# Kernel tuning notes

Hardware: AMD Instinct MI355X
Metric: run time of the kernel (lower is better)

The kernel has to match this reference:

```python
import jax, jax.numpy as jnp
import numpy as np

B, V, N, C, H = 4, 8, 256, 768, 12
DH = C // H
NEG = -1e9


def setup_inputs() -> dict:
    key = jax.random.key(0)
    k0, k1, k2, k3, k4, k5 = jax.random.split(key, 6)
    feats = jax.random.normal(k0, (B, V, N, C), dtype=jnp.float32)
    is_ref = jax.random.randint(k1, (B, V), 0, 2).astype(bool)
    # nn.MultiheadAttention params: packed in_proj (3C, C) + bias, out_proj Linear(C, C)
    w_qkv = jax.random.normal(k2, (3 * C, C), dtype=jnp.float32) * 0.02
    b_qkv = jax.random.normal(k3, (3 * C,), dtype=jnp.float32) * 0.02
    w_out = jax.random.normal(k4, (C, C), dtype=jnp.float32) * 0.02
    b_out = jax.random.normal(k5, (C,), dtype=jnp.float32) * 0.02
    return {"feats": feats, "is_ref": is_ref, "w_qkv": w_qkv, "b_qkv": b_qkv,
            "w_out": w_out, "b_out": b_out}


def reference(feats, is_ref, w_qkv, b_qkv, w_out, b_out):
    b_, v_, n_, c_ = feats.shape
    # packed QKV projection (torch Linear: x @ W.T + b)
    qkv = feats @ w_qkv.T + b_qkv                      # (B,V,N,3C)
    q, k, v = jnp.split(qkv, 3, axis=-1)
    q = q.reshape(b_, v_, n_, H, DH) * (1.0 / jnp.sqrt(jnp.float32(DH)))
    k = k.reshape(b_, v_ * n_, H, DH)                  # keys flattened over views
    v = v.reshape(b_, v_ * n_, H, DH)
    # view v attends to views w with opposite ref flag
    allowed = is_ref[:, :, None] ^ is_ref[:, None, :]  # (B,V,V) bool
    key_mask = jnp.repeat(allowed, n_, axis=2)         # (B,V,V*N)
    scores = jnp.einsum('bvnhd,bmhd->bhvnm', q, k)     # (B,H,V,N,V*N)
    logits = jnp.where(key_mask[:, None, :, None, :], scores, NEG)
    attn = jax.nn.softmax(logits, axis=-1)
    ctx = jnp.einsum('bhvnm,bmhd->bvnhd', attn, v).reshape(b_, v_, n_, c_)
    out = ctx @ w_out.T + b_out
    # views with empty context pass through unchanged
    has_ctx = allowed.any(axis=-1)                     # (B,V)
    return jnp.where(has_ctx[:, :, None, None], out, feats)
```

## Files before the change

### kernel.cpp

```cpp
#include <hip/hip_runtime.h>
#include <hip/hip_bf16.h>
#include <math.h>

#define BDIM 4
#define VDIM 8
#define NDIM 256
#define CDIM 768
#define HDIM 12
#define DHE  64
#define C3   (3*CDIM)
#define ROWS (BDIM*VDIM*NDIM)
#define KEYS (VDIM*NDIM)

typedef __attribute__((ext_vector_type(8))) short short8;
typedef __attribute__((ext_vector_type(4))) float float4v;

__device__ inline unsigned short f2bf(float f) {
    unsigned int u = __builtin_bit_cast(unsigned int, f);
    u += 0x7fffu + ((u >> 16) & 1u);
    return (unsigned short)(u >> 16);
}

__device__ __forceinline__ unsigned int pk2(float a, float b) {
    return (unsigned int)f2bf(a) | ((unsigned int)f2bf(b) << 16);
}

__device__ __forceinline__ uint4 pk8(float4 a, float4 b) {
    uint4 r;
    r.x = pk2(a.x, a.y); r.y = pk2(a.z, a.w);
    r.z = pk2(b.x, b.y); r.w = pk2(b.z, b.w);
    return r;
}

__device__ __forceinline__ void gld_lds16(const unsigned short* g, unsigned short* l) {
    __builtin_amdgcn_global_load_lds(
        (const __attribute__((address_space(1))) void*)g,
        (__attribute__((address_space(3))) void*)l, 16, 0, 0);
}

#define NA8 786432
#define NW8 221184
#define NO8 73728

__global__ __launch_bounds__(256) void cast_bf16_all(
    const float* __restrict__ fA, const float* __restrict__ fW,
    const float* __restrict__ fO,
    unsigned short* __restrict__ bA, unsigned short* __restrict__ bW,
    unsigned short* __restrict__ bO)
{
    const int gid = blockIdx.x * 256 + threadIdx.x;
    const float* src;
    unsigned short* dst;
    int idx;
    if (gid < NA8)            { src = fA; dst = bA; idx = gid; }
    else if (gid < NA8 + NW8) { src = fW; dst = bW; idx = gid - NA8; }
    else                      { src = fO; dst = bO; idx = gid - NA8 - NW8; }
    const float4* p = (const float4*)(src + (size_t)idx * 8);
    *(uint4*)(dst + (size_t)idx * 8) = pk8(p[0], p[1]);
}

__global__ __launch_bounds__(256) void gemm_qkv_mfma(
    const unsigned short* __restrict__ A,
    const unsigned short* __restrict__ W,
    const float* __restrict__ bias,
    unsigned short* __restrict__ out,
    unsigned short* __restrict__ vT)
{
    __shared__ __attribute__((aligned(16))) unsigned short As[128][32];
    __shared__ __attribute__((aligned(16))) unsigned short Ws[128][32];
    const int t = threadIdx.x;
    const int wave = t >> 6, lane = t & 63;
    const int m = lane & 15, quad = lane >> 4;
    const int wr = (wave >> 1) * 64, wc = (wave & 1) * 64;
    const int row0 = blockIdx.y * 128, col0 = blockIdx.x * 128;

    const int sr = t >> 2, sk = (t & 3) * 8;
    const unsigned short* ag = &A[(size_t)(row0 + sr) * CDIM + sk];
    const unsigned short* wg = &W[(size_t)(col0 + sr) * CDIM + sk];
    unsigned short* la0 = &As[sr][sk];
    unsigned short* la1 = &As[64 + sr][sk];
    unsigned short* lw0 = &Ws[sr][sk];
    unsigned short* lw1 = &Ws[64 + sr][sk];

    float4v acc[4][4] = {};

    for (int k0 = 0; k0 < CDIM; k0 += 32) {
        gld_lds16(ag + k0, la0);
        gld_lds16(ag + (size_t)64 * CDIM + k0, la1);
        gld_lds16(wg + k0, lw0);
        gld_lds16(wg + (size_t)64 * CDIM + k0, lw1);
        __syncthreads();
        short8 a[4], b[4];
        #pragma unroll
        for (int rt = 0; rt < 4; rt++)
            a[rt] = *(const short8*)&As[wr + rt * 16 + m][quad * 8];
        #pragma unroll
        for (int ct = 0; ct < 4; ct++)
            b[ct] = *(const short8*)&Ws[wc + ct * 16 + m][quad * 8];
        #pragma unroll
        for (int rt = 0; rt < 4; rt++)
            #pragma unroll
            for (int ct = 0; ct < 4; ct++)
                acc[rt][ct] = __builtin_amdgcn_mfma_f32_16x16x32_bf16(
                    a[rt], b[ct], acc[rt][ct], 0, 0, 0);
        __syncthreads();
    }

    if (col0 < 2 * CDIM) {
        #pragma unroll
        for (int ct = 0; ct < 4; ct++) {
            const int col = col0 + wc + ct * 16 + m;
            const float bv = bias[col];
            #pragma unroll
            for (int rt = 0; rt < 4; rt++) {
                const size_t row = (size_t)row0 + wr + rt * 16 + quad * 4;
                #pragma unroll
                for (int r = 0; r < 4; r++)
                    out[(row + r) * C3 + col] = f2bf(acc[rt][ct][r] + bv);
            }
        }
    } else {
        #pragma unroll
        for (int ct = 0; ct < 4; ct++) {
            const int vcol = col0 + wc + ct * 16 + m - 2 * CDIM;
            const int h = vcol >> 6, d = vcol & 63;
            const float bv = bias[col0 + wc + ct * 16 + m];
            #pragma unroll
            for (int rt = 0; rt < 4; rt++) {
                const int row = row0 + wr + rt * 16 + quad * 4;
                const int bidx = row >> 11, key = row & 2047;
                ushort4 pkv;
                pkv.x = f2bf(acc[rt][ct][0] + bv);
                pkv.y = f2bf(acc[rt][ct][1] + bv);
                pkv.z = f2bf(acc[rt][ct][2] + bv);
                pkv.w = f2bf(acc[rt][ct][3] + bv);
                *(ushort4*)&vT[((size_t)(bidx * HDIM + h) * DHE + d) * KEYS + key] = pkv;
            }
        }
    }
}

__global__ __launch_bounds__(256, 3) void attn_mfma(
    const unsigned short* __restrict__ qkv,
    const unsigned short* __restrict__ vT,
    const int* __restrict__ is_ref,
    unsigned short* __restrict__ ctx)
{
    const int g = blockIdx.x;
    const int myx = g & 7, cuu = (g >> 3) & 31, round = g >> 8;
    const int j = round * 32 + ((round & 1) ? (31 - cuu) : cuu);

    int rmask[4], r4[4];
    #pragma unroll
    for (int bb = 0; bb < 4; bb++) {
        int mask = 0;
        #pragma unroll
        for (int w = 0; w < VDIM; w++)
            if (is_ref[bb * VDIM + w] != 0) mask |= 1 << w;
        rmask[bb] = mask; r4[bb] = __popc(mask);
    }
    int ord[4] = {0, 1, 2, 3};
    #pragma unroll
    for (int i = 0; i < 3; i++)
        #pragma unroll
        for (int k = 0; k < 3 - i; k++) {
            const int wa = r4[ord[k]] * (8 - r4[ord[k]]);
            const int wb = r4[ord[k + 1]] * (8 - r4[ord[k + 1]]);
            if (wb > wa) { int tmp = ord[k]; ord[k] = ord[k + 1]; ord[k + 1] = tmp; }
        }
    int Gb[6], Gh[6], ng = 0;
    for (int p = 0; p < 48; p++) {
        const int row = p >> 3, col = p & 7;
        const int x = (row & 1) ? (7 - col) : col;
        if (x == myx) { Gb[ng] = ord[p / 12]; Gh[ng] = p % 12; ng++; }
    }
    int b = 0, h = 0, half = 0, v = 0, Lsel = 0;
    {
        int jj = j;
        bool found = false;
        for (int o = 8; o >= 0 && !found; o--) {
            for (int gi = 0; gi < 6 && !found; gi++) {
                const int b2 = Gb[gi], r2 = r4[b2];
                const int nv_o = ((8 - r2) == o ? r2 : 0) + (r2 == o ? (8 - r2) : 0);
                const int cnt = 2 * nv_o;
                if (cnt > 0 && jj < cnt) {
                    b = b2; h = Gh[gi]; Lsel = o;
                    half = jj / nv_o;
                    int pos = jj % nv_o;
                    int S = (((8 - r2) == o) ? rmask[b2] : 0)
                          | ((r2 == o) ? ((~rmask[b2]) & 0xff) : 0);
                    for (int vv = 0; vv < 8; vv++)
                        if ((S >> vv) & 1) { if (pos == 0) { v = vv; break; } pos--; }
                    found = true;
                } else jj -= cnt;
            }
        }
    }

    const int t = threadIdx.x, wave = t >> 6, lane = t & 63;
    const int m = lane & 15, quad = lane >> 4;
    const int n0 = half * 128 + wave * 32;

    __shared__ unsigned short Ks[128][64];
    __shared__ unsigned short Vs[64][128];
    __shared__ unsigned short Ps[4][32][72];

    const int my_ref = (rmask[b] >> v) & 1;
    const unsigned amask = my_ref ? (unsigned)((~rmask[b]) & 0xff)
                                  : (unsigned)rmask[b];
    const int nChunks = 2 * Lsel;

    const float c1 = 0.18033688f;

    short8 aq[2][2];
    #pragma unroll
    for (int qt = 0; qt < 2; qt++) {
        const size_t row = (size_t)((b * VDIM + v) * NDIM) + n0 + qt * 16 + m;
        #pragma unroll
        for (int ks = 0; ks < 2; ks++)
            aq[qt][ks] = *(const short8*)&qkv[row * C3 + h * DHE + ks * 32 + quad * 8];
    }

    float rs[2] = {0.f, 0.f};
    float4v O[2][4] = {};

    const int k_key = t >> 3, k_dg = t & 7;
    const int v_dim = t >> 4, v_kg = t & 15;

    const unsigned short* vTb = vT + (size_t)(b * HDIM + h) * DHE * KEYS;

    uint4 kreg[4], vreg[4];
    unsigned rem2 = amask;
    int wcur = __builtin_ffs((int)rem2) - 1;

    if (nChunks > 0) {
        const unsigned short* kb =
            qkv + (size_t)((b * VDIM + wcur) * NDIM) * C3 + CDIM + h * DHE;
        #pragma unroll
        for (int i = 0; i < 4; i++)
            kreg[i] = *(const uint4*)&kb[(size_t)(i * 32 + k_key) * C3 + k_dg * 8];
        #pragma unroll
        for (int i = 0; i < 4; i++)
            vreg[i] = *(const uint4*)&vTb[(size_t)(i * 16 + v_dim) * KEYS
                                          + wcur * NDIM + v_kg * 8];
    }

    for (int ci = 0; ci < nChunks; ci++) {
        __syncthreads();
        #pragma unroll
        for (int i = 0; i < 4; i++)
            *(uint4*)&Ks[i * 32 + k_key][(k_dg ^ (k_key & 7)) * 8] = kreg[i];
        #pragma unroll
        for (int i = 0; i < 4; i++)
            *(uint4*)&Vs[i * 16 + v_dim][(v_kg ^ v_dim) * 8] = vreg[i];

        if (ci + 1 < nChunks) {
            int wn, m0n;
            if ((ci & 1) == 0) { wn = wcur; m0n = 128; }
            else {
                unsigned r2 = rem2 & (rem2 - 1);
                wn = __builtin_ffs((int)r2) - 1; m0n = 0;
            }
            const unsigned short* kb =
                qkv + (size_t)((b * VDIM + wn) * NDIM + m0n) * C3 + CDIM + h * DHE;
            #pragma unroll
            for (int i = 0; i < 4; i++)
                kreg[i] = *(const uint4*)&kb[(size_t)(i * 32 + k_key) * C3 + k_dg * 8];
            #pragma unroll
            for (int i = 0; i < 4; i++)
                vreg[i] = *(const uint4*)&vTb[(size_t)(i * 16 + v_dim) * KEYS
                                              + wn * NDIM + m0n + v_kg * 8];
        }
        __syncthreads();

        #pragma unroll
        for (int hk = 0; hk < 2; hk++) {
            #pragma unroll
            for (int kt = 0; kt < 4; kt++) {
                const int nt = hk * 4 + kt;
                const short8 bk0 = *(const short8*)&Ks[nt * 16 + m][(quad ^ (m & 7)) * 8];
                const short8 bk1 = *(const short8*)&Ks[nt * 16 + m][((4 + quad) ^ (m & 7)) * 8];
                #pragma unroll
                for (int qt = 0; qt < 2; qt++) {
                    float4v s = {};
                    s = __builtin_amdgcn_mfma_f32_16x16x32_bf16(bk0, aq[qt][0], s, 0, 0, 0);
                    s = __builtin_amdgcn_mfma_f32_16x16x32_bf16(bk1, aq[qt][1], s, 0, 0, 0);
                    const float p0 = __builtin_amdgcn_exp2f(s[0] * c1);
                    const float p1 = __builtin_amdgcn_exp2f(s[1] * c1);
                    const float p2 = __builtin_amdgcn_exp2f(s[2] * c1);
                    const float p3 = __builtin_amdgcn_exp2f(s[3] * c1);
                    rs[qt] += (p0 + p1) + (p2 + p3);
                    uint2 pw;
                    pw.x = pk2(p0, p1);
                    pw.y = pk2(p2, p3);
                    *(uint2*)&Ps[wave][qt * 16 + m][kt * 16 + quad * 4] = pw;
                }
            }
            #pragma unroll
            for (int kk = 0; kk < 2; kk++) {
                const short8 ap0 = *(const short8*)&Ps[wave][m][kk * 32 + quad * 8];
                const short8 ap1 = *(const short8*)&Ps[wave][16 + m][kk * 32 + quad * 8];
                #pragma unroll
                for (int ct = 0; ct < 4; ct++) {
                    const short8 bv = *(const short8*)&Vs[ct * 16 + m]
                        [((hk * 8 + kk * 4 + quad) ^ m) * 8];
                    O[0][ct] = __builtin_amdgcn_mfma_f32_16x16x32_bf16(ap0, bv, O[0][ct], 0, 0, 0);
                    O[1][ct] = __builtin_amdgcn_mfma_f32_16x16x32_bf16(ap1, bv, O[1][ct], 0, 0, 0);
                }
            }
        }
        if (ci & 1) { rem2 &= rem2 - 1; wcur = __builtin_ffs((int)rem2) - 1; }
    }

    #pragma unroll
    for (int qt = 0; qt < 2; qt++) {
        float x = rs[qt];
        x += __shfl_xor(x, 16, 64);
        x += __shfl_xor(x, 32, 64);
        const float inv = (x > 0.f) ? 1.f / x : 0.f;
        float invq[4];
        #pragma unroll
        for (int r = 0; r < 4; r++)
            invq[r] = __shfl(inv, quad * 4 + r, 64);
        const size_t rowg = (size_t)((b * VDIM + v) * NDIM) + n0 + qt * 16 + quad * 4;
        #pragma unroll
        for (int ct = 0; ct < 4; ct++)
            #pragma unroll
            for (int r = 0; r < 4; r++)
                ctx[(rowg + r) * CDIM + h * DHE + ct * 16 + m] = f2bf(O[qt][ct][r] * invq[r]);
    }
}

__global__ __launch_bounds__(256) void gemm_out_mfma(
    const unsigned short* __restrict__ A,
    const unsigned short* __restrict__ W,
    const float* __restrict__ bias,
    const float* __restrict__ feats,
    const int* __restrict__ is_ref,
    float* __restrict__ out)
{
    __shared__ __attribute__((aligned(16))) unsigned short As[128][32];
    __shared__ __attribute__((aligned(16))) unsigned short Ws[128][32];
    const int t = threadIdx.x;
    const int wave = t >> 6, lane = t & 63;
    const int m = lane & 15, quad = lane >> 4;
    const int wr = (wave >> 1) * 64, wc = (wave & 1) * 64;
    const int row0 = blockIdx.y * 128, col0 = blockIdx.x * 128;

    const int sr = t >> 2, sk = (t & 3) * 8;
    const unsigned short* ag = &A[(size_t)(row0 + sr) * CDIM + sk];
    const unsigned short* wg = &W[(size_t)(col0 + sr) * CDIM + sk];
    unsigned short* la0 = &As[sr][sk];
    unsigned short* la1 = &As[64 + sr][sk];
    unsigned short* lw0 = &Ws[sr][sk];
    unsigned short* lw1 = &Ws[64 + sr][sk];

    float4v acc[4][4] = {};

    for (int k0 = 0; k0 < CDIM; k0 += 32) {
        gld_lds16(ag + k0, la0);
        gld_lds16(ag + (size_t)64 * CDIM + k0, la1);
        gld_lds16(wg + k0, lw0);
        gld_lds16(wg + (size_t)64 * CDIM + k0, lw1);
        __syncthreads();
        short8 a[4], b[4];
        #pragma unroll
        for (int rt = 0; rt < 4; rt++)
            a[rt] = *(const short8*)&As[wr + rt * 16 + m][quad * 8];
        #pragma unroll
        for (int ct = 0; ct < 4; ct++)
            b[ct] = *(const short8*)&Ws[wc + ct * 16 + m][quad * 8];
        #pragma unroll
        for (int rt = 0; rt < 4; rt++)
            #pragma unroll
            for (int ct = 0; ct < 4; ct++)
                acc[rt][ct] = __builtin_amdgcn_mfma_f32_16x16x32_bf16(
                    a[rt], b[ct], acc[rt][ct], 0, 0, 0);
        __syncthreads();
    }

    const int bidx = row0 / (VDIM * NDIM);
    const int vidx = (row0 / NDIM) % VDIM;
    const int my = is_ref[bidx * VDIM + vidx];
    bool has = false;
    #pragma unroll
    for (int w = 0; w < VDIM; w++) has = has || (is_ref[bidx * VDIM + w] != my);

    #pragma unroll
    for (int ct = 0; ct < 4; ct++) {
        const int col = col0 + wc + ct * 16 + m;
        const float bv = bias[col];
        #pragma unroll
        for (int rt = 0; rt < 4; rt++) {
            const size_t row = (size_t)row0 + wr + rt * 16 + quad * 4;
            #pragma unroll
            for (int r = 0; r < 4; r++) {
                float o = acc[rt][ct][r] + bv;
                if (!has) o = feats[(row + r) * CDIM + col];
                out[(row + r) * CDIM + col] = o;
            }
        }
    }
}

extern "C" void kernel_launch(void* const* d_in, const int* in_sizes, int n_in,
                              void* d_out, int out_size, void* d_ws, size_t ws_size,
                              hipStream_t stream) {
    const float* feats = (const float*)d_in[0];
    const int*   is_ref = (const int*)d_in[1];
    const float* w_qkv = (const float*)d_in[2];
    const float* b_qkv = (const float*)d_in[3];
    const float* w_out = (const float*)d_in[4];
    const float* b_out = (const float*)d_in[5];
    float* out = (float*)d_out;

    unsigned short* qkv_b = (unsigned short*)d_ws;
    unsigned short* vT    = qkv_b + (size_t)ROWS * C3;
    unsigned short* ctx_b = vT + (size_t)BDIM * HDIM * DHE * KEYS;
    unsigned short* A_bf  = ctx_b + (size_t)ROWS * CDIM;
    unsigned short* Wq_bf = A_bf + (size_t)ROWS * CDIM;
    unsigned short* Wo_bf = Wq_bf + (size_t)C3 * CDIM;

    cast_bf16_all<<<dim3((NA8 + NW8 + NO8) / 256), 256, 0, stream>>>(
        feats, w_qkv, w_out, A_bf, Wq_bf, Wo_bf);

    dim3 g1(C3 / 128, ROWS / 128);
    gemm_qkv_mfma<<<g1, 256, 0, stream>>>(A_bf, Wq_bf, b_qkv, qkv_b, vT);

    attn_mfma<<<dim3(768), 256, 0, stream>>>(qkv_b, vT, is_ref, ctx_b);

    dim3 g3(CDIM / 128, ROWS / 128);
    gemm_out_mfma<<<g3, 256, 0, stream>>>(ctx_b, Wo_bf, b_out, feats, is_ref, out);
    (void)in_sizes; (void)n_in; (void)out_size; (void)ws_size;
}
```

Before: 245.9 us.

## Swizzle GEMM block order per XCD and pass P via lane shuffles instead of LDS

```diff
diff --git a/kernel.cpp b/kernel.cpp
--- a/kernel.cpp
+++ b/kernel.cpp
@@ -72,7 +72,11 @@
     const int wave = t >> 6, lane = t & 63;
     const int m = lane & 15, quad = lane >> 4;
     const int wr = (wave >> 1) * 64, wc = (wave & 1) * 64;
-    const int row0 = blockIdx.y * 128, col0 = blockIdx.x * 128;
+
+    const int lin = blockIdx.y * gridDim.x + blockIdx.x;
+    const int cpx = (gridDim.x * gridDim.y) >> 3;
+    const int swz = (lin & 7) * cpx + (lin >> 3);
+    const int row0 = (swz / gridDim.x) * 128, col0 = (swz % gridDim.x) * 128;
 
     const int sr = t >> 2, sk = (t & 3) * 8;
     const unsigned short* ag = &A[(size_t)(row0 + sr) * CDIM + sk];
@@ -203,7 +207,6 @@
 
     __shared__ unsigned short Ks[128][64];
     __shared__ unsigned short Vs[64][128];
-    __shared__ unsigned short Ps[4][32][72];
 
     const int my_ref = (rmask[b] >> v) & 1;
     const unsigned amask = my_ref ? (unsigned)((~rmask[b]) & 0xff)
@@ -226,6 +229,10 @@
 
     const int k_key = t >> 3, k_dg = t & 7;
     const int v_dim = t >> 4, v_kg = t & 15;
+
+    const int src0 = ((quad & 1) << 5) + m;
+    const int src1 = src0 + 16;
+    const bool hiq = (quad >> 1) != 0;
 
     const unsigned short* vTb = vT + (size_t)(b * HDIM + h) * DHE * KEYS;
 
@@ -275,6 +282,7 @@
 
         #pragma unroll
         for (int hk = 0; hk < 2; hk++) {
+            uint2 pq[2][4];
             #pragma unroll
             for (int kt = 0; kt < 4; kt++) {
                 const int nt = hk * 4 + kt;
@@ -290,16 +298,30 @@
                     const float p2 = __builtin_amdgcn_exp2f(s[2] * c1);
                     const float p3 = __builtin_amdgcn_exp2f(s[3] * c1);
                     rs[qt] += (p0 + p1) + (p2 + p3);
-                    uint2 pw;
-                    pw.x = pk2(p0, p1);
-                    pw.y = pk2(p2, p3);
-                    *(uint2*)&Ps[wave][qt * 16 + m][kt * 16 + quad * 4] = pw;
+                    pq[qt][kt].x = pk2(p0, p1);
+                    pq[qt][kt].y = pk2(p2, p3);
                 }
             }
             #pragma unroll
             for (int kk = 0; kk < 2; kk++) {
-                const short8 ap0 = *(const short8*)&Ps[wave][m][kk * 32 + quad * 8];
-                const short8 ap1 = *(const short8*)&Ps[wave][16 + m][kk * 32 + quad * 8];
+                uint4 u[2];
+                #pragma unroll
+                for (int qt = 0; qt < 2; qt++) {
+                    const unsigned lox  = __shfl(pq[qt][kk * 2].x,     src0);
+                    const unsigned loy  = __shfl(pq[qt][kk * 2].y,     src0);
+                    const unsigned hix  = __shfl(pq[qt][kk * 2 + 1].x, src0);
+                    const unsigned hiy  = __shfl(pq[qt][kk * 2 + 1].y, src0);
+                    const unsigned lox1 = __shfl(pq[qt][kk * 2].x,     src1);
+                    const unsigned loy1 = __shfl(pq[qt][kk * 2].y,     src1);
+                    const unsigned hix1 = __shfl(pq[qt][kk * 2 + 1].x, src1);
+                    const unsigned hiy1 = __shfl(pq[qt][kk * 2 + 1].y, src1);
+                    u[qt].x = hiq ? hix  : lox;
+                    u[qt].y = hiq ? hiy  : loy;
+                    u[qt].z = hiq ? hix1 : lox1;
+                    u[qt].w = hiq ? hiy1 : loy1;
+                }
+                const short8 ap0 = __builtin_bit_cast(short8, u[0]);
+                const short8 ap1 = __builtin_bit_cast(short8, u[1]);
                 #pragma unroll
                 for (int ct = 0; ct < 4; ct++) {
                     const short8 bv = *(const short8*)&Vs[ct * 16 + m]
@@ -345,7 +367,11 @@
     const int wave = t >> 6, lane = t & 63;
     const int m = lane & 15, quad = lane >> 4;
     const int wr = (wave >> 1) * 64, wc = (wave & 1) * 64;
-    const int row0 = blockIdx.y * 128, col0 = blockIdx.x * 128;
+
+    const int lin = blockIdx.y * gridDim.x + blockIdx.x;
+    const int cpx = (gridDim.x * gridDim.y) >> 3;
+    const int swz = (lin & 7) * cpx + (lin >> 3);
+    const int row0 = (swz / gridDim.x) * 128, col0 = (swz % gridDim.x) * 128;
 
     const int sr = t >> 2, sk = (t & 3) * 8;
     const unsigned short* ag = &A[(size_t)(row0 + sr) * CDIM + sk];
```

Measured after the change: 244.1 us. About the same (-0.7%).
